# Kernel optimization log

Hardware: AMD Instinct MI355X
Metric: run time of the kernel (lower is better)

## Reference

```python
import jax, jax.numpy as jnp
import numpy as np

S = 256
H = 4       # n_heads
DH = 32     # head_dim
D = H * DH  # model dim
EPS = 1e-5


def setup_inputs() -> dict:
    key = jax.random.key(0)
    ks = jax.random.split(key, 12)
    x = jax.random.normal(ks[0], (1, S, S, D), dtype=jnp.float32)
    # attention mask: mostly 0, occasionally large negative (masked)
    keep = jax.random.uniform(ks[1], (1, 1, S, S)) < 0.9
    attn_mask = jnp.where(keep, 0.0, -1e9).astype(jnp.float32)
    sc = 1.0 / np.sqrt(D)
    ln_w = jnp.ones((D,), jnp.float32)
    ln_b = jnp.zeros((D,), jnp.float32)
    Wb = jax.random.normal(ks[2], (H, D), jnp.float32) * sc   # bias projection (linear.weight)
    Wq = jax.random.normal(ks[3], (D, D), jnp.float32) * sc
    Wk = jax.random.normal(ks[4], (D, D), jnp.float32) * sc
    Wv = jax.random.normal(ks[5], (D, D), jnp.float32) * sc
    Wg = jax.random.normal(ks[6], (D, D), jnp.float32) * sc
    Wo = jax.random.normal(ks[7], (D, D), jnp.float32) * sc
    return {"x": x, "attn_mask": attn_mask, "ln_w": ln_w, "ln_b": ln_b,
            "Wb": Wb, "Wq": Wq, "Wk": Wk, "Wv": Wv, "Wg": Wg, "Wo": Wo}


def reference(x, attn_mask, ln_w, ln_b, Wb, Wq, Wk, Wv, Wg, Wo):
    # x: [1,S,S,D] pair representation; ending=False so no transpose of S axes.
    x0 = x[0]  # [S,S,D]
    mu = jnp.mean(x0, axis=-1, keepdims=True)
    var = jnp.mean(jnp.square(x0 - mu), axis=-1, keepdims=True)
    xn = (x0 - mu) * jax.lax.rsqrt(var + EPS) * ln_w + ln_b  # [S,S,D]

    # triangle bias: [S,S,H] -> [1,H,S,S] (broadcast over batch-of-rows)
    bias = jnp.einsum('bqd,hd->hbq', xn, Wb)[None]  # [1,H,S,S]

    def heads(W):
        return jnp.einsum('bqd,ed->bqe', xn, W).reshape(S, S, H, DH).transpose(0, 2, 1, 3)

    q, k, v = heads(Wq), heads(Wk), heads(Wv)  # each [S,H,S,DH]

    scale = 1.0 / np.sqrt(DH)
    scores = jnp.einsum('bhqd,bhkd->bhqk', q, k) * scale + bias + attn_mask  # [S,H,S,S]
    attn = jax.nn.softmax(scores, axis=-1)
    o = jnp.einsum('bhqk,bhkd->bhqd', attn, v)  # [S,H,S,DH]
    o = o.transpose(0, 2, 1, 3).reshape(S, S, D)

    g = jnp.einsum('bqd,ed->bqe', xn, Wg)
    out = jnp.einsum('bqe,fe->bqf', o * jax.nn.sigmoid(g), Wo)  # [S,S,D]
    return out[None]  # [1,S,S,D]
```

## Files before the change

kernel.cpp:

```cpp
#include <hip/hip_runtime.h>
#include <hip/hip_bf16.h>

#define S_DIM 256
#define D_DIM 128
#define H_DIM 4
#define NPOS  (S_DIM * S_DIM)
#define SW    384
#define LOG2E 1.4426950408889634f

typedef __attribute__((ext_vector_type(8))) short  short8;
typedef __attribute__((ext_vector_type(4))) float  f32x4;

__device__ __forceinline__ float b2f(unsigned short u) {
    union { float f; unsigned int u32; } c; c.u32 = ((unsigned int)u) << 16; return c.f;
}
__device__ __forceinline__ unsigned short f2b(float f) {
    __hip_bfloat16 h = __float2bfloat16(f);
    return *reinterpret_cast<unsigned short*>(&h);
}

__global__ __launch_bounds__(256) void wconv_kernel(
    const float* __restrict__ Wq, const float* __restrict__ Wk,
    const float* __restrict__ Wv, const float* __restrict__ Wg,
    const float* __restrict__ Wo, unsigned short* __restrict__ wbf)
{
    const int gy = blockIdx.y;
    const float* W = (gy == 0) ? Wq : (gy == 1) ? Wk : (gy == 2) ? Wv
                   : (gy == 3) ? Wg : Wo;
    const int idx = (blockIdx.x * 256 + threadIdx.x) * 8;
    float4 f0 = *(const float4*)(W + idx);
    float4 f1 = *(const float4*)(W + idx + 4);
    unsigned short pk[8] = {f2b(f0.x), f2b(f0.y), f2b(f0.z), f2b(f0.w),
                            f2b(f1.x), f2b(f1.y), f2b(f1.z), f2b(f1.w)};
    *(uint4*)(wbf + (size_t)gy * 16384 + idx) = *(const uint4*)pk;
}

__global__ __launch_bounds__(256) void ln_biasmask_kernel(
    const float* __restrict__ x, const float* __restrict__ mask,
    const float* __restrict__ lnw, const float* __restrict__ lnb,
    const float* __restrict__ Wb, float* __restrict__ bm)
{
    const int wave = threadIdx.x >> 6, lane = threadIdx.x & 63;
    const int p = blockIdx.x * 4 + wave;

    float2 v = ((const float2*)x)[p * 64 + lane];
    float s = v.x + v.y, ss = v.x * v.x + v.y * v.y;
    #pragma unroll
    for (int m = 1; m < 64; m <<= 1) { s += __shfl_xor(s, m); ss += __shfl_xor(ss, m); }
    float mean = s * (1.f / 128.f);
    float var  = ss * (1.f / 128.f) - mean * mean;
    float rstd = rsqrtf(var + 1e-5f);

    float xn0 = (v.x - mean) * rstd * lnw[lane * 2]     + lnb[lane * 2];
    float xn1 = (v.y - mean) * rstd * lnw[lane * 2 + 1] + lnb[lane * 2 + 1];

    float mval = mask[p];
    #pragma unroll
    for (int h = 0; h < H_DIM; h++) {
        float d = xn0 * Wb[h * 128 + lane * 2] + xn1 * Wb[h * 128 + lane * 2 + 1];
        #pragma unroll
        for (int m = 1; m < 64; m <<= 1) d += __shfl_xor(d, m);
        if (lane == 0) bm[(long)h * NPOS + p] = (d + mval) * LOG2E;
    }
}

template<int FUSE_BIAS>
__global__ __launch_bounds__(256) void proj_ln_kernel(
    const float* __restrict__ x, const float* __restrict__ mask,
    const float* __restrict__ lnw, const float* __restrict__ lnb,
    const float* __restrict__ Wb, const unsigned short* __restrict__ wbf,
    int p0, unsigned short* __restrict__ strip, unsigned short* __restrict__ vt,
    float* __restrict__ bm)
{
    __shared__ __align__(16) unsigned short A_lds[64 * 136];
    __shared__ __align__(16) unsigned short W_lds[128 * 136];
    const int tid = threadIdx.x;
    const int m0 = blockIdx.x * 64;
    const int lr = tid >> 4, c8 = (tid & 15) * 8;

    float4 wb0[4], wb1[4];
    if (FUSE_BIAS) {
        #pragma unroll
        for (int hh = 0; hh < 4; hh++) {
            wb0[hh] = *(const float4*)(Wb + hh * 128 + c8);
            wb1[hh] = *(const float4*)(Wb + hh * 128 + c8 + 4);
        }
    }

    #pragma unroll
    for (int i = 0; i < 4; i++) {
        int row = lr + i * 16;
        int p   = p0 + m0 + row;
        const float* src = x + (size_t)p * 128 + c8;
        float4 f0 = *(const float4*)(src);
        float4 f1 = *(const float4*)(src + 4);
        float s  = f0.x + f0.y + f0.z + f0.w + f1.x + f1.y + f1.z + f1.w;
        float ss = f0.x*f0.x + f0.y*f0.y + f0.z*f0.z + f0.w*f0.w
                 + f1.x*f1.x + f1.y*f1.y + f1.z*f1.z + f1.w*f1.w;
        #pragma unroll
        for (int m = 1; m < 16; m <<= 1) { s += __shfl_xor(s, m); ss += __shfl_xor(ss, m); }
        float mean = s * (1.f / 128.f);
        float var  = ss * (1.f / 128.f) - mean * mean;
        float rstd = rsqrtf(var + 1e-5f);
        float xv[8] = {f0.x, f0.y, f0.z, f0.w, f1.x, f1.y, f1.z, f1.w};
        float xl[8];
        unsigned short pk[8];
        #pragma unroll
        for (int j = 0; j < 8; j++) {
            xl[j] = (xv[j] - mean) * rstd * lnw[c8 + j] + lnb[c8 + j];
            pk[j] = f2b(xl[j]);
        }
        *(uint4*)(&A_lds[row * 136 + c8]) = *(const uint4*)pk;

        if (FUSE_BIAS) {
            float mv = 0.f;
            if ((tid & 15) == 0) mv = mask[p];
            #pragma unroll
            for (int hh = 0; hh < 4; hh++) {
                float bh = xl[0]*wb0[hh].x + xl[1]*wb0[hh].y
                         + xl[2]*wb0[hh].z + xl[3]*wb0[hh].w
                         + xl[4]*wb1[hh].x + xl[5]*wb1[hh].y
                         + xl[6]*wb1[hh].z + xl[7]*wb1[hh].w;
                #pragma unroll
                for (int mk = 1; mk < 16; mk <<= 1) bh += __shfl_xor(bh, mk);
                if ((tid & 15) == 0) bm[(long)hh * NPOS + p] = (bh + mv) * LOG2E;
            }
        }
    }
    __syncthreads();

    const int w = tid >> 6, lane = tid & 63;
    const int l16 = lane & 15, quad = lane >> 4;

    short8 a4[4];
    #pragma unroll
    for (int k0i = 0; k0i < 4; k0i++)
        a4[k0i] = *(const short8*)(&A_lds[(w * 16 + l16) * 136 + k0i * 32 + quad * 8]);

    #pragma unroll 1
    for (int gy = 0; gy < 4; gy++) {
        if (gy > 0) __syncthreads();
        const uint4* wsrc = (const uint4*)(wbf + (size_t)gy * 16384);
        #pragma unroll
        for (int j = 0; j < 8; j++) {
            int idx = tid + j * 256;
            int row = idx >> 4, cc = (idx & 15) * 8;
            *(uint4*)(&W_lds[row * 136 + cc]) = wsrc[idx];
        }
        __syncthreads();

        f32x4 acc[8];
        #pragma unroll
        for (int nt = 0; nt < 8; nt++) acc[nt] = (f32x4){0.f, 0.f, 0.f, 0.f};

        if (gy == 2) {
            #pragma unroll
            for (int k0i = 0; k0i < 4; k0i++)
                #pragma unroll
                for (int nt = 0; nt < 8; nt++) {
                    short8 b = *(const short8*)(&W_lds[(nt * 16 + l16) * 136 + k0i * 32 + quad * 8]);
                    acc[nt] = __builtin_amdgcn_mfma_f32_16x16x32_bf16(a4[k0i], b, acc[nt], 0, 0, 0);
                }
            const int blv = m0 >> 8;
            const int kl  = (m0 & 255) + w * 16 + quad * 4;
            #pragma unroll
            for (int nt = 0; nt < 8; nt++) {
                uint2 pk;
                pk.x = (unsigned)f2b(acc[nt][0]) | ((unsigned)f2b(acc[nt][1]) << 16);
                pk.y = (unsigned)f2b(acc[nt][2]) | ((unsigned)f2b(acc[nt][3]) << 16);
                *(uint2*)(&vt[((size_t)(blv * 128 + nt * 16 + l16)) * 256 + kl]) = pk;
            }
        } else {
            #pragma unroll
            for (int k0i = 0; k0i < 4; k0i++)
                #pragma unroll
                for (int nt = 0; nt < 8; nt++) {
                    short8 b = *(const short8*)(&W_lds[(nt * 16 + l16) * 136 + k0i * 32 + quad * 8]);
                    acc[nt] = __builtin_amdgcn_mfma_f32_16x16x32_bf16(b, a4[k0i], acc[nt], 0, 0, 0);
                }
            const int off = (gy == 0) ? 0 : (gy == 1) ? 128 : 256;
            const size_t rowbase = (size_t)(m0 + w * 16 + l16) * SW + off;
            #pragma unroll
            for (int nt = 0; nt < 8; nt++) {
                uint2 pk;
                pk.x = (unsigned)f2b(acc[nt][0]) | ((unsigned)f2b(acc[nt][1]) << 16);
                pk.y = (unsigned)f2b(acc[nt][2]) | ((unsigned)f2b(acc[nt][3]) << 16);
                *(uint2*)(&strip[rowbase + nt * 16 + quad * 4]) = pk;
            }
        }
    }
}

__global__ __launch_bounds__(64) void attn_kernel(
    const unsigned short* __restrict__ strip, const unsigned short* __restrict__ vt,
    const float* __restrict__ bm, int b0, unsigned short* __restrict__ gated)
{
    const int bl = blockIdx.x, h = blockIdx.y, z = blockIdx.z;
    const int b  = b0 + bl;
    const int lane = threadIdx.x & 63;
    const int l16 = lane & 15, quad = lane >> 4;
    const float* bmh = bm + (long)h * NPOS;
    const unsigned short* vth = vt + ((size_t)bl * 128 + h * 32) * 256;
    const float scale2 = 0.17677669529663687f * LOG2E;

    #pragma unroll 1
    for (int i = 0; i < 4; i++) {
        const int q0 = (z * 4 + i) * 16;
        short8 bq = *(const short8*)(strip + (size_t)(bl * 256 + q0 + l16) * SW + h * 32 + quad * 8);
        const float* brow = bmh + (size_t)(q0 + l16) * 256 + quad * 4;

        float sc[16][4];
        #pragma unroll
        for (int nt = 0; nt < 16; nt++) {
            short8 ka = *(const short8*)(strip + (size_t)(bl * 256 + nt * 16 + l16) * SW + 128 + h * 32 + quad * 8);
            f32x4 c = (f32x4){0.f, 0.f, 0.f, 0.f};
            c = __builtin_amdgcn_mfma_f32_16x16x32_bf16(ka, bq, c, 0, 0, 0);
            float4 bb = *(const float4*)(brow + nt * 16);
            sc[nt][0] = c[0] * scale2 + bb.x;
            sc[nt][1] = c[1] * scale2 + bb.y;
            sc[nt][2] = c[2] * scale2 + bb.z;
            sc[nt][3] = c[3] * scale2 + bb.w;
        }

        float m0_ = sc[0][0], m1_ = sc[0][1], m2_ = sc[0][2], m3_ = sc[0][3];
        #pragma unroll
        for (int nt = 1; nt < 16; nt++) {
            m0_ = fmaxf(m0_, sc[nt][0]); m1_ = fmaxf(m1_, sc[nt][1]);
            m2_ = fmaxf(m2_, sc[nt][2]); m3_ = fmaxf(m3_, sc[nt][3]);
        }
        float m = fmaxf(fmaxf(m0_, m1_), fmaxf(m2_, m3_));
        m = fmaxf(m, __shfl_xor(m, 16));
        m = fmaxf(m, __shfl_xor(m, 32));

        float s0 = 0.f, s1 = 0.f, s2 = 0.f, s3 = 0.f;
        f32x4 oacc[2];
        oacc[0] = (f32x4){0.f, 0.f, 0.f, 0.f};
        oacc[1] = (f32x4){0.f, 0.f, 0.f, 0.f};
        #pragma unroll
        for (int kt = 0; kt < 8; kt++) {
            const int na = kt * 2, nb = kt * 2 + 1;
            float e0 = exp2f(sc[na][0] - m); s0 += e0;
            float e1 = exp2f(sc[na][1] - m); s1 += e1;
            float e2 = exp2f(sc[na][2] - m); s2 += e2;
            float e3 = exp2f(sc[na][3] - m); s3 += e3;
            float f0_ = exp2f(sc[nb][0] - m); s0 += f0_;
            float f1_ = exp2f(sc[nb][1] - m); s1 += f1_;
            float f2_ = exp2f(sc[nb][2] - m); s2 += f2_;
            float f3_ = exp2f(sc[nb][3] - m); s3 += f3_;
            union { unsigned int u[4]; short8 s; } pu;
            pu.u[0] = (unsigned)f2b(e0)  | ((unsigned)f2b(e1)  << 16);
            pu.u[1] = (unsigned)f2b(e2)  | ((unsigned)f2b(e3)  << 16);
            pu.u[2] = (unsigned)f2b(f0_) | ((unsigned)f2b(f1_) << 16);
            pu.u[3] = (unsigned)f2b(f2_) | ((unsigned)f2b(f3_) << 16);
            short8 pa = pu.s;
            #pragma unroll
            for (int nh = 0; nh < 2; nh++) {
                const unsigned short* vrow = vth + (size_t)(nh * 16 + l16) * 256 + kt * 32 + quad * 4;
                uint2 vlo = *(const uint2*)(vrow);
                uint2 vhi = *(const uint2*)(vrow + 16);
                union { unsigned int u[4]; short8 s; } vu;
                vu.u[0] = vlo.x; vu.u[1] = vlo.y;
                vu.u[2] = vhi.x; vu.u[3] = vhi.y;
                oacc[nh] = __builtin_amdgcn_mfma_f32_16x16x32_bf16(pa, vu.s, oacc[nh], 0, 0, 0);
            }
        }
        float ssum = (s0 + s1) + (s2 + s3);
        ssum += __shfl_xor(ssum, 16);
        ssum += __shfl_xor(ssum, 32);
        float inv = 1.f / ssum;

        #pragma unroll
        for (int rr = 0; rr < 4; rr++) {
            float invr = __shfl(inv, quad * 4 + rr);
            int row = q0 + quad * 4 + rr;
            #pragma unroll
            for (int nh = 0; nh < 2; nh++) {
                int cl = nh * 16 + l16;
                float g = b2f(strip[(size_t)(bl * 256 + row) * SW + 256 + h * 32 + cl]);
                float ov = oacc[nh][rr] * invr;
                ov = ov / (1.f + __expf(-g));
                gated[((size_t)b * 256 + row) * 128 + h * 32 + cl] = f2b(ov);
            }
        }
    }
}

__global__ __launch_bounds__(256) void outproj_mfma_kernel(
    const unsigned short* __restrict__ gated, const unsigned short* __restrict__ wbf,
    float* __restrict__ out)
{
    const int tid = threadIdx.x, m0 = blockIdx.x * 64;
    const int w = tid >> 6, lane = tid & 63;
    const int l16 = lane & 15, quad = lane >> 4;
    const unsigned short* Wo = wbf + (size_t)4 * 16384;

    const unsigned short* arow = gated + (size_t)(m0 + w * 16 + l16) * 128;
    short8 a4[4];
    #pragma unroll
    for (int k0i = 0; k0i < 4; k0i++)
        a4[k0i] = *(const short8*)(arow + k0i * 32 + quad * 8);

    f32x4 acc[8];
    #pragma unroll
    for (int nt = 0; nt < 8; nt++) acc[nt] = (f32x4){0.f, 0.f, 0.f, 0.f};

    #pragma unroll
    for (int k0i = 0; k0i < 4; k0i++)
        #pragma unroll
        for (int nt = 0; nt < 8; nt++) {
            short8 b = *(const short8*)(Wo + (size_t)(nt * 16 + l16) * 128 + k0i * 32 + quad * 8);
            acc[nt] = __builtin_amdgcn_mfma_f32_16x16x32_bf16(b, a4[k0i], acc[nt], 0, 0, 0);
        }

    float* orow = out + (size_t)(m0 + w * 16 + l16) * 128;
    #pragma unroll
    for (int nt = 0; nt < 8; nt++)
        *(f32x4*)(&orow[nt * 16 + quad * 4]) = acc[nt];
}

extern "C" void kernel_launch(void* const* d_in, const int* in_sizes, int n_in,
                              void* d_out, int out_size, void* d_ws, size_t ws_size,
                              hipStream_t stream)
{
    (void)in_sizes; (void)n_in; (void)out_size;
    const float* x    = (const float*)d_in[0];
    const float* mask = (const float*)d_in[1];
    const float* lnw  = (const float*)d_in[2];
    const float* lnb  = (const float*)d_in[3];
    const float* Wb   = (const float*)d_in[4];
    const float* Wq   = (const float*)d_in[5];
    const float* Wk   = (const float*)d_in[6];
    const float* Wv   = (const float*)d_in[7];
    const float* Wg   = (const float*)d_in[8];
    const float* Wo   = (const float*)d_in[9];
    float* out = (float*)d_out;

    const size_t bmB = (size_t)H_DIM * NPOS * sizeof(float);
    const size_t gB  = (size_t)NPOS * 128 * sizeof(unsigned short);
    const size_t wB  = (size_t)5 * 16384 * sizeof(unsigned short);
    const size_t perRow = (size_t)256 * SW * 2 + (size_t)128 * 256 * 2;
    int HB = 256;
    while (HB > 16 && bmB + gB + wB + (size_t)HB * perRow > ws_size) HB >>= 1;

    char* ws = (char*)d_ws;
    float*          bm    = (float*)ws;
    unsigned short* gated = (unsigned short*)(ws + bmB);
    unsigned short* wbf   = (unsigned short*)(ws + bmB + gB);
    unsigned short* vt    = (unsigned short*)(ws + bmB + gB + wB);
    unsigned short* strip = vt + (size_t)HB * 128 * 256;

    wconv_kernel<<<dim3(8, 5), 256, 0, stream>>>(Wq, Wk, Wv, Wg, Wo, wbf);

    if (HB == 256) {
        proj_ln_kernel<1><<<dim3(256 * 4), 256, 0, stream>>>(
            x, mask, lnw, lnb, Wb, wbf, 0, strip, vt, bm);
        attn_kernel<<<dim3(256, H_DIM, 4), 64, 0, stream>>>(strip, vt, bm, 0, gated);
    } else {
        ln_biasmask_kernel<<<NPOS / 4, 256, 0, stream>>>(x, mask, lnw, lnb, Wb, bm);
        for (int b0 = 0; b0 < S_DIM; b0 += HB) {
            proj_ln_kernel<0><<<dim3(HB * 4), 256, 0, stream>>>(
                x, mask, lnw, lnb, Wb, wbf, b0 * 256, strip, vt, bm);
            attn_kernel<<<dim3(HB, H_DIM, 4), 64, 0, stream>>>(strip, vt, bm, b0, gated);
        }
    }
    outproj_mfma_kernel<<<NPOS / 64, 256, 0, stream>>>(gated, wbf, out);
}
```

Before: 235.8 us.

## Fuse output projection into attention kernel via LDS-staged gated tile

Merges the attention and output-projection kernels. One 1024-thread block now handles a whole row b across all 4 heads. The gated output goes into LDS instead of global memory, and Wo is staged in LDS so the final GEMM runs in-block. This drops the global write and read of the gated intermediate and one launch. In exchange the grid is much coarser (256 blocks of 16 waves), LDS use per block is large (about 104KB), and there is a block-wide barrier, which may cut occupancy and latency hiding.

```diff
diff --git a/kernel.cpp b/kernel.cpp
--- a/kernel.cpp
+++ b/kernel.cpp
@@ -191,21 +191,37 @@
     }
 }
 
-__global__ __launch_bounds__(64) void attn_kernel(
+__global__ __launch_bounds__(1024) void attn_fused_kernel(
     const unsigned short* __restrict__ strip, const unsigned short* __restrict__ vt,
-    const float* __restrict__ bm, int b0, unsigned short* __restrict__ gated)
-{
-    const int bl = blockIdx.x, h = blockIdx.y, z = blockIdx.z;
+    const float* __restrict__ bm, const unsigned short* __restrict__ wbf,
+    int b0, float* __restrict__ out)
+{
+    __shared__ __align__(16) unsigned short G_lds[256 * 136];
+    __shared__ __align__(16) unsigned short Wo_lds[128 * 136];
+    const int bl = blockIdx.x;
     const int b  = b0 + bl;
-    const int lane = threadIdx.x & 63;
+    const int tid = threadIdx.x;
+    const int w = tid >> 6, lane = tid & 63;
+    const int h  = w >> 2;
+    const int wq = w & 3;
     const int l16 = lane & 15, quad = lane >> 4;
     const float* bmh = bm + (long)h * NPOS;
     const unsigned short* vth = vt + ((size_t)bl * 128 + h * 32) * 256;
     const float scale2 = 0.17677669529663687f * LOG2E;
 
+    {
+        const uint4* wsrc = (const uint4*)(wbf + (size_t)4 * 16384);
+        #pragma unroll
+        for (int j = 0; j < 2; j++) {
+            int idx = tid + j * 1024;
+            int row = idx >> 4, cc = (idx & 15) * 8;
+            *(uint4*)(&Wo_lds[row * 136 + cc]) = wsrc[idx];
+        }
+    }
+
     #pragma unroll 1
     for (int i = 0; i < 4; i++) {
-        const int q0 = (z * 4 + i) * 16;
+        const int q0 = (wq * 4 + i) * 16;
         short8 bq = *(const short8*)(strip + (size_t)(bl * 256 + q0 + l16) * SW + h * 32 + quad * 8);
         const float* brow = bmh + (size_t)(q0 + l16) * 256 + quad * 4;
 
@@ -279,26 +295,18 @@
                 float g = b2f(strip[(size_t)(bl * 256 + row) * SW + 256 + h * 32 + cl]);
                 float ov = oacc[nh][rr] * invr;
                 ov = ov / (1.f + __expf(-g));
-                gated[((size_t)b * 256 + row) * 128 + h * 32 + cl] = f2b(ov);
-            }
-        }
-    }
-}
-
-__global__ __launch_bounds__(256) void outproj_mfma_kernel(
-    const unsigned short* __restrict__ gated, const unsigned short* __restrict__ wbf,
-    float* __restrict__ out)
-{
-    const int tid = threadIdx.x, m0 = blockIdx.x * 64;
-    const int w = tid >> 6, lane = tid & 63;
-    const int l16 = lane & 15, quad = lane >> 4;
-    const unsigned short* Wo = wbf + (size_t)4 * 16384;
-
-    const unsigned short* arow = gated + (size_t)(m0 + w * 16 + l16) * 128;
+                G_lds[row * 136 + h * 32 + cl] = f2b(ov);
+            }
+        }
+    }
+
+    __syncthreads();
+
+    const int orow = w * 16 + l16;
     short8 a4[4];
     #pragma unroll
     for (int k0i = 0; k0i < 4; k0i++)
-        a4[k0i] = *(const short8*)(arow + k0i * 32 + quad * 8);
+        a4[k0i] = *(const short8*)(&G_lds[orow * 136 + k0i * 32 + quad * 8]);
 
     f32x4 acc[8];
     #pragma unroll
@@ -308,14 +316,14 @@
     for (int k0i = 0; k0i < 4; k0i++)
         #pragma unroll
         for (int nt = 0; nt < 8; nt++) {
-            short8 b = *(const short8*)(Wo + (size_t)(nt * 16 + l16) * 128 + k0i * 32 + quad * 8);
-            acc[nt] = __builtin_amdgcn_mfma_f32_16x16x32_bf16(b, a4[k0i], acc[nt], 0, 0, 0);
-        }
-
-    float* orow = out + (size_t)(m0 + w * 16 + l16) * 128;
+            short8 bw = *(const short8*)(&Wo_lds[(nt * 16 + l16) * 136 + k0i * 32 + quad * 8]);
+            acc[nt] = __builtin_amdgcn_mfma_f32_16x16x32_bf16(bw, a4[k0i], acc[nt], 0, 0, 0);
+        }
+
+    float* orowp = out + ((size_t)b * 256 + orow) * 128;
     #pragma unroll
     for (int nt = 0; nt < 8; nt++)
-        *(f32x4*)(&orow[nt * 16 + quad * 4]) = acc[nt];
+        *(f32x4*)(&orowp[nt * 16 + quad * 4]) = acc[nt];
 }
 
 extern "C" void kernel_launch(void* const* d_in, const int* in_sizes, int n_in,
@@ -336,17 +344,15 @@
     float* out = (float*)d_out;
 
     const size_t bmB = (size_t)H_DIM * NPOS * sizeof(float);
-    const size_t gB  = (size_t)NPOS * 128 * sizeof(unsigned short);
     const size_t wB  = (size_t)5 * 16384 * sizeof(unsigned short);
     const size_t perRow = (size_t)256 * SW * 2 + (size_t)128 * 256 * 2;
     int HB = 256;
-    while (HB > 16 && bmB + gB + wB + (size_t)HB * perRow > ws_size) HB >>= 1;
+    while (HB > 16 && bmB + wB + (size_t)HB * perRow > ws_size) HB >>= 1;
 
     char* ws = (char*)d_ws;
     float*          bm    = (float*)ws;
-    unsigned short* gated = (unsigned short*)(ws + bmB);
-    unsigned short* wbf   = (unsigned short*)(ws + bmB + gB);
-    unsigned short* vt    = (unsigned short*)(ws + bmB + gB + wB);
+    unsigned short* wbf   = (unsigned short*)(ws + bmB);
+    unsigned short* vt    = (unsigned short*)(ws + bmB + wB);
     unsigned short* strip = vt + (size_t)HB * 128 * 256;
 
     wconv_kernel<<<dim3(8, 5), 256, 0, stream>>>(Wq, Wk, Wv, Wg, Wo, wbf);
@@ -354,14 +360,13 @@
     if (HB == 256) {
         proj_ln_kernel<1><<<dim3(256 * 4), 256, 0, stream>>>(
             x, mask, lnw, lnb, Wb, wbf, 0, strip, vt, bm);
-        attn_kernel<<<dim3(256, H_DIM, 4), 64, 0, stream>>>(strip, vt, bm, 0, gated);
+        attn_fused_kernel<<<dim3(256), 1024, 0, stream>>>(strip, vt, bm, wbf, 0, out);
     } else {
         ln_biasmask_kernel<<<NPOS / 4, 256, 0, stream>>>(x, mask, lnw, lnb, Wb, bm);
         for (int b0 = 0; b0 < S_DIM; b0 += HB) {
             proj_ln_kernel<0><<<dim3(HB * 4), 256, 0, stream>>>(
                 x, mask, lnw, lnb, Wb, wbf, b0 * 256, strip, vt, bm);
-            attn_kernel<<<dim3(HB, H_DIM, 4), 64, 0, stream>>>(strip, vt, bm, b0, gated);
-        }
-    }
-    outproj_mfma_kernel<<<NPOS / 64, 256, 0, stream>>>(gated, wbf, out);
-}
+            attn_fused_kernel<<<dim3(HB), 1024, 0, stream>>>(strip, vt, bm, wbf, b0, out);
+        }
+    }
+}
```

New measurement: 256.1 us. 8.6% more time.
